# Kernel tuning notes

Measured on AMD Instinct MI355X. Metric: run time of the kernel, lower is better.

## Reference

```python
import jax, jax.numpy as jnp
import numpy as np

B, N, E, T = 32768, 6, 6, 2  # batch graphs, nodes, edges (ring), edge types
H, DIN = 128, 3


def _ring_rel():
    # off_diag[i, (i+1)%N] = 1 -> edge e: sender i, receiver (i+1)%N
    send = np.arange(N)
    recv = (np.arange(N) + 1) % N
    eye = np.eye(N, dtype=np.float32)
    return jnp.asarray(eye[recv]), jnp.asarray(eye[send])  # rel_rec, rel_send [E,N]


def setup_inputs() -> dict:
    key = jax.random.key(0)
    ks = iter(jax.random.split(key, 40))
    rn = lambda shape, s=0.1: jax.random.normal(next(ks), shape, jnp.float32) * s
    rel_rec, rel_send = _ring_rel()
    inp = {
        'x': rn((B, N, DIN), 1.0),
        'rel_rec': rel_rec, 'rel_send': rel_send,
        'e1w1': rn((DIN, H)), 'e1b1': jnp.full((H,), 0.1), 'e1w2': rn((H, H)), 'e1b2': jnp.full((H,), 0.1),
        'e2w1': rn((2 * H, H)), 'e2b1': jnp.full((H,), 0.1), 'e2w2': rn((H, H)), 'e2b2': jnp.full((H,), 0.1),
        'e3w1': rn((H, H)), 'e3b1': jnp.full((H,), 0.1), 'e3w2': rn((H, H)), 'e3b2': jnp.full((H,), 0.1),
        'e4w1': rn((2 * H, H)), 'e4b1': jnp.full((H,), 0.1), 'e4w2': rn((H, H)), 'e4b2': jnp.full((H,), 0.1),
        'ew_out': rn((H, T)), 'eb_out': jnp.full((T,), 0.1),
        'd_msg_w1': rn((T, 2 * DIN, H)), 'd_msg_b1': rn((T, H), 0.01),
        'd_msg_w2': rn((T, H, H)), 'd_msg_b2': rn((T, H), 0.01),
        'd_out_w1': rn((DIN + H, H)), 'd_out_b1': rn((H,), 0.01),
        'd_out_w2': rn((H, H)), 'd_out_b2': rn((H,), 0.01),
        'd_out_w3': rn((H, DIN)), 'd_out_b3': rn((DIN,), 0.01),
    }
    return inp


def _mlp(h, w1, b1, w2, b2):
    # two-layer ELU MLP (dropout inactive at eval)
    return jax.nn.elu(jax.nn.elu(h @ w1 + b1) @ w2 + b2)


def reference(x, rel_rec, rel_send,
              e1w1, e1b1, e1w2, e1b2, e2w1, e2b1, e2w2, e2b2,
              e3w1, e3b1, e3w2, e3b2, e4w1, e4b1, e4w2, e4b2,
              ew_out, eb_out,
              d_msg_w1, d_msg_b1, d_msg_w2, d_msg_b2,
              d_out_w1, d_out_b1, d_out_w2, d_out_b2, d_out_w3, d_out_b3):
    node2edge = lambda h: jnp.concatenate(
        [jnp.einsum('en,bnh->beh', rel_rec, h), jnp.einsum('en,bnh->beh', rel_send, h)], axis=-1)

    # ---- GraphEncoder (factor=False) ----
    h = _mlp(x, e1w1, e1b1, e1w2, e1b2)                      # [B,N,H]
    he = _mlp(node2edge(h), e2w1, e2b1, e2w2, e2b2)          # [B,E,H]
    h2 = _mlp(he, e3w1, e3b1, e3w2, e3b2)                    # [B,E,H]
    h3 = _mlp(jnp.concatenate([h2, he], -1), e4w1, e4b1, e4w2, e4b2)
    logits = h3 @ ew_out + eb_out                            # [B,E,T]
    rel_type = jax.nn.softmax(logits, axis=-1)               # edge-type weights

    # ---- GraphDecoder single step (skip_first=False) ----
    recv = jnp.einsum('en,bnd->bed', rel_rec, x)             # [B,E,DIN]
    send = jnp.einsum('en,bnd->bed', rel_send, x)
    pre_msg = jnp.concatenate([recv, send], axis=-1)         # [B,E,2*DIN]
    # batched per-edge-type MLP: one grouped GEMM instead of a python loop of layers
    m = jax.nn.relu(jnp.einsum('bei,tih->bteh', pre_msg, d_msg_w1) + d_msg_b1[None, :, None, :])
    m = jax.nn.relu(jnp.einsum('bteh,tho->bteo', m, d_msg_w2) + d_msg_b2[None, :, None, :])
    all_msgs = jnp.einsum('bteh,bet->beh', m, rel_type)      # weight + accumulate over types
    agg_msgs = jnp.einsum('beh,en->bnh', all_msgs, rel_rec)  # edge -> node aggregation

    aug = jnp.concatenate([x, agg_msgs], axis=-1)            # [B,N,DIN+H]
    p = jax.nn.relu(aug @ d_out_w1 + d_out_b1)
    p = jax.nn.relu(p @ d_out_w2 + d_out_b2)
    p = p @ d_out_w3 + d_out_b3
    return x + p                                             # [B,N,DIN]
```

## Files before the change

kernel.cpp:

```cpp
#include <hip/hip_runtime.h>
#include <hip/hip_bf16.h>

typedef __bf16 bf16x8 __attribute__((ext_vector_type(8)));
typedef __bf16 bf16x4 __attribute__((ext_vector_type(4)));
typedef float floatx4 __attribute__((ext_vector_type(4)));

#define LDW 136
#define PXW 8

#define O_E1W2  0
#define O_E2W1  16384
#define O_E2W2  49152
#define O_E3W1  65536
#define O_E3W2  81920
#define O_E4W1  98304
#define O_E4W2  131072
#define O_DM2T0 147456
#define O_DM2T1 163840
#define O_DO1   180224
#define O_DO2   196608
#define O_EWOUT 212992
#define O_DW3   215040
#define O_E1W1P 217088
#define O_M1T0P 221184
#define O_M1T1P 225280
#define O_DO1XP 229376
#define WS_ELEMS 233472

__global__ void prep_kernel(const float* e1w2, const float* e2w1, const float* e2w2,
    const float* e3w1, const float* e3w2, const float* e4w1, const float* e4w2,
    const float* dmsg2, const float* dout1, const float* dout2,
    const float* ew_out, const float* dout_w3, const float* e1w1,
    const float* dmsg_w1, __hip_bfloat16* ws) {
  int idx = blockIdx.x * 256 + threadIdx.x;
  if (idx >= WS_ELEMS) return;
  float v;
  if (idx < O_E2W1)      { int l = idx;           v = e1w2[(l & 127) * 128 + (l >> 7)]; }
  else if (idx < O_E2W2) { int l = idx - O_E2W1;  v = e2w1[(l & 255) * 128 + (l >> 8)]; }
  else if (idx < O_E3W1) { int l = idx - O_E2W2;  v = e2w2[(l & 127) * 128 + (l >> 7)]; }
  else if (idx < O_E3W2) { int l = idx - O_E3W1;  v = e3w1[(l & 127) * 128 + (l >> 7)]; }
  else if (idx < O_E4W1) { int l = idx - O_E3W2;  v = e3w2[(l & 127) * 128 + (l >> 7)]; }
  else if (idx < O_E4W2) { int l = idx - O_E4W1;  v = e4w1[(l & 255) * 128 + (l >> 8)]; }
  else if (idx < O_DM2T0){ int l = idx - O_E4W2;  v = e4w2[(l & 127) * 128 + (l >> 7)]; }
  else if (idx < O_DM2T1){ int l = idx - O_DM2T0; v = dmsg2[(l & 127) * 128 + (l >> 7)]; }
  else if (idx < O_DO1)  { int l = idx - O_DM2T1; v = dmsg2[16384 + (l & 127) * 128 + (l >> 7)]; }
  else if (idx < O_DO2)  { int l = idx - O_DO1;   v = dout1[384 + (l & 127) * 128 + (l >> 7)]; }
  else if (idx < O_EWOUT){ int l = idx - O_DO2;   v = dout2[(l & 127) * 128 + (l >> 7)]; }
  else if (idx < O_DW3)  { int l = idx - O_EWOUT; int n = l >> 7;
                           v = (n < 2) ? ew_out[(l & 127) * 2 + n] : 0.f; }
  else if (idx < O_E1W1P){ int l = idx - O_DW3;   int n = l >> 7;
                           v = (n < 3) ? dout_w3[(l & 127) * 3 + n] : 0.f; }
  else if (idx < O_M1T0P){ int l = idx - O_E1W1P; int n = l >> 5, c = l & 31;
                           v = (c >= 3 && c < 6) ? e1w1[(c - 3) * 128 + n] : 0.f; }
  else if (idx < O_M1T1P){ int l = idx - O_M1T0P; int n = l >> 5, c = l & 31;
                           v = (c < 6) ? dmsg_w1[c * 128 + n] : 0.f; }
  else if (idx < O_DO1XP){ int l = idx - O_M1T1P; int n = l >> 5, c = l & 31;
                           v = (c < 6) ? dmsg_w1[768 + c * 128 + n] : 0.f; }
  else                   { int l = idx - O_DO1XP; int n = l >> 5, c = l & 31;
                           v = (c >= 3 && c < 6) ? dout1[(c - 3) * 128 + n] : 0.f; }
  ws[idx] = __float2bfloat16(v);
}

struct W4 { bf16x8 b[4]; };
struct W8 { bf16x8 b[8]; };
union PK { bf16x4 v; __hip_bfloat16 h[4]; };

__global__ __launch_bounds__(512, 4) void nri_fused(
    const float* __restrict__ x,
    const float* __restrict__ e1b1, const float* __restrict__ e1b2,
    const float* __restrict__ e2b1, const float* __restrict__ e2b2,
    const float* __restrict__ e3b1, const float* __restrict__ e3b2,
    const float* __restrict__ e4b1, const float* __restrict__ e4b2,
    const float* __restrict__ eb_out,
    const float* __restrict__ dmsg_b1, const float* __restrict__ dmsg_b2,
    const float* __restrict__ dout_b1, const float* __restrict__ dout_b2,
    const float* __restrict__ dout_b3,
    const __bf16* __restrict__ wt, float* __restrict__ out)
{
  const int tid  = threadIdx.x;
  const int wave = tid >> 6;
  const int lane = tid & 63;
  const int nl   = lane & 15;
  const int quad = lane >> 4;
  const int colb = wave * 16 + nl;
  const int cq   = wave * 16 + quad * 4;
  const int gx   = blockIdx.x * 288;

  __shared__ __align__(16) __hip_bfloat16 bufA[96 * LDW];
  __shared__ __align__(16) __hip_bfloat16 bufB[96 * LDW];
  __shared__ __align__(16) __hip_bfloat16 pxb[96 * PXW];
  __shared__ __hip_bfloat16 rtw[192];

  floatx4 b_s1 = *(const floatx4*)(e1b1 + cq);
  bf16x8 wk_s1 = *(const bf16x8*)(wt + O_E1W1P + colb * 32 + quad * 8);

  for (int i = tid; i < 96 * PXW; i += 512) {
    int row = i >> 3, c = i & 7;
    int e = row % 6;
    float v = 0.f;
    if (c < 3)      { int rr = row + ((e == 5) ? -5 : 1); v = x[gx + rr * 3 + c]; }
    else if (c < 6) v = x[gx + row * 3 + (c - 3)];
    pxb[i] = __float2bfloat16(v);
  }
  __syncthreads();

  auto initv = [&](floatx4 (&a)[6], floatx4 bv) {
#pragma unroll
    for (int mt = 0; mt < 6; ++mt) a[mt] = bv;
  };

  auto loadW128 = [&](int wofs) {
    W4 w;
    const __bf16* p = wt + wofs + colb * 128 + quad * 8;
#pragma unroll
    for (int ks = 0; ks < 4; ++ks) w.b[ks] = *(const bf16x8*)(p + ks * 32);
    return w;
  };
  auto loadW256 = [&](int wofs) {
    W8 w;
    const __bf16* p = wt + wofs + colb * 256 + quad * 8;
#pragma unroll
    for (int ks = 0; ks < 8; ++ks) w.b[ks] = *(const bf16x8*)(p + ks * 32);
    return w;
  };
  auto loadW256half = [&](int wofs, int kh) {
    W4 w;
    const __bf16* p = wt + wofs + colb * 256 + kh * 128 + quad * 8;
#pragma unroll
    for (int ks = 0; ks < 4; ++ks) w.b[ks] = *(const bf16x8*)(p + ks * 32);
    return w;
  };

  auto gemmP = [&](floatx4 (&acc)[6], const W4& w, const __hip_bfloat16* in) {
    const __bf16* ab = (const __bf16*)(const void*)in;
#pragma unroll
    for (int ks = 0; ks < 4; ++ks) {
      int kk = ks * 32 + quad * 8;
#pragma unroll
      for (int mt = 0; mt < 6; ++mt) {
        bf16x8 b = *(const bf16x8*)(ab + (mt * 16 + nl) * LDW + kk);
        acc[mt] = __builtin_amdgcn_mfma_f32_16x16x32_bf16(w.b[ks], b, acc[mt], 0, 0, 0);
      }
    }
  };
  auto gemmP2 = [&](floatx4 (&accA)[6], const W4& wA, floatx4 (&accB)[6],
                    const W4& wB, const __hip_bfloat16* in) {
    const __bf16* ab = (const __bf16*)(const void*)in;
#pragma unroll
    for (int ks = 0; ks < 4; ++ks) {
      int kk = ks * 32 + quad * 8;
#pragma unroll
      for (int mt = 0; mt < 6; ++mt) {
        bf16x8 b = *(const bf16x8*)(ab + (mt * 16 + nl) * LDW + kk);
        accA[mt] = __builtin_amdgcn_mfma_f32_16x16x32_bf16(wA.b[ks], b, accA[mt], 0, 0, 0);
        accB[mt] = __builtin_amdgcn_mfma_f32_16x16x32_bf16(wB.b[ks], b, accB[mt], 0, 0, 0);
      }
    }
  };
  auto gemm256P = [&](floatx4 (&acc)[6], const W8& w, const __hip_bfloat16* in) {
    int rofs0[6], rofs1[6];
#pragma unroll
    for (int mt = 0; mt < 6; ++mt) {
      int r = mt * 16 + nl;
      rofs1[mt] = r * LDW;
      int e = r % 6;
      rofs0[mt] = (r + ((e == 5) ? -5 : 1)) * LDW;
    }
    const __bf16* ab = (const __bf16*)(const void*)in;
#pragma unroll
    for (int ks = 0; ks < 8; ++ks) {
      int kk = (ks & 3) * 32 + quad * 8;
      const int* rofs = (ks < 4) ? rofs0 : rofs1;
#pragma unroll
      for (int mt = 0; mt < 6; ++mt) {
        bf16x8 b = *(const bf16x8*)(ab + rofs[mt] + kk);
        acc[mt] = __builtin_amdgcn_mfma_f32_16x16x32_bf16(w.b[ks], b, acc[mt], 0, 0, 0);
      }
    }
  };
  auto gemm32 = [&](floatx4 (&acc)[6], bf16x8 wfrag) {
    const __bf16* pb = (const __bf16*)(const void*)pxb;
#pragma unroll
    for (int mt = 0; mt < 6; ++mt) {
      bf16x8 b = {0, 0, 0, 0, 0, 0, 0, 0};
      if (quad == 0) b = *(const bf16x8*)(pb + (mt * 16 + nl) * PXW);
      acc[mt] = __builtin_amdgcn_mfma_f32_16x16x32_bf16(wfrag, b, acc[mt], 0, 0, 0);
    }
  };
  auto store_act = [&](floatx4 (&acc)[6], int act, __hip_bfloat16* ob) {
#pragma unroll
    for (int mt = 0; mt < 6; ++mt) {
      PK p;
#pragma unroll
      for (int r = 0; r < 4; ++r) {
        float z = acc[mt][r];
        if (act == 1) z = (z > 0.f) ? z : (__expf(z) - 1.f);
        else z = fmaxf(z, 0.f);
        p.h[r] = __float2bfloat16(z);
      }
      *(bf16x4*)((__bf16*)(void*)ob + (mt * 16 + nl) * LDW + cq) = p.v;
    }
  };

  floatx4 acc[6], acc2[6];

  initv(acc, b_s1); gemm32(acc, wk_s1);
  W4 w2 = loadW128(O_E1W2);
  floatx4 b_s2 = *(const floatx4*)(e1b2 + cq);
  store_act(acc, 1, bufA);
  __syncthreads();
  initv(acc, b_s2); gemmP(acc, w2, bufA);
  W8 w3 = loadW256(O_E2W1);
  floatx4 b_s3 = *(const floatx4*)(e2b1 + cq);
  store_act(acc, 1, bufB);
  __syncthreads();
  initv(acc, b_s3); gemm256P(acc, w3, bufB);
  W4 w4 = loadW128(O_E2W2);
  floatx4 b_s4 = *(const floatx4*)(e2b2 + cq);
  store_act(acc, 1, bufA);
  __syncthreads();
  initv(acc, b_s4); gemmP(acc, w4, bufA);
  W4 w5 = loadW128(O_E3W1);
  W4 w5b = loadW256half(O_E4W1, 1);
  floatx4 b_s5 = *(const floatx4*)(e3b1 + cq);
  floatx4 b2_s5 = *(const floatx4*)(e4b1 + cq);
  store_act(acc, 1, bufB);
  __syncthreads();
  initv(acc, b_s5); initv(acc2, b2_s5);
  gemmP2(acc, w5, acc2, w5b, bufB);
  W4 w6 = loadW128(O_E3W2);
  floatx4 b_s6 = *(const floatx4*)(e3b2 + cq);
  store_act(acc, 1, bufA);
  __syncthreads();
  initv(acc, b_s6); gemmP(acc, w6, bufA);
  W4 w7 = loadW256half(O_E4W1, 0);
  store_act(acc, 1, bufB);
  __syncthreads();
  gemmP(acc2, w7, bufB);
  W4 w8 = loadW128(O_E4W2);
  floatx4 b_s8 = *(const floatx4*)(e4b2 + cq);
  store_act(acc2, 1, bufA);
  __syncthreads();
  initv(acc, b_s8); gemmP(acc, w8, bufA);
  float ebv = (nl < 2) ? eb_out[nl] : 0.f;
  bf16x8 wk10a = *(const bf16x8*)(wt + O_M1T0P + colb * 32 + quad * 8);
  bf16x8 wk10b = *(const bf16x8*)(wt + O_M1T1P + colb * 32 + quad * 8);
  floatx4 b_m0 = *(const floatx4*)(dmsg_b1 + cq);
  floatx4 b_m1 = *(const floatx4*)(dmsg_b1 + 128 + cq);
  store_act(acc, 1, bufB);
  __syncthreads();

  if (wave < 6) {
    int tile = wave;
    floatx4 lg = {ebv, ebv, ebv, ebv};
    const __bf16* ab = (const __bf16*)(const void*)bufB;
    const __bf16* wp = wt + O_EWOUT + nl * 128 + quad * 8;
#pragma unroll
    for (int ks = 0; ks < 4; ++ks) {
      bf16x8 a = *(const bf16x8*)(ab + (tile * 16 + nl) * LDW + ks * 32 + quad * 8);
      bf16x8 b = *(const bf16x8*)(wp + ks * 32);
      lg = __builtin_amdgcn_mfma_f32_16x16x32_bf16(a, b, lg, 0, 0, 0);
    }
    if (nl < 2) {
#pragma unroll
      for (int r = 0; r < 4; ++r)
        rtw[(tile * 16 + quad * 4 + r) * 2 + nl] = __float2bfloat16(lg[r]);
    }
  }
  __syncthreads();

  if (tid < 96) {
    float l0 = __bfloat162float(rtw[tid * 2]);
    float l1 = __bfloat162float(rtw[tid * 2 + 1]);
    float mx = fmaxf(l0, l1);
    float ea = __expf(l0 - mx), eb = __expf(l1 - mx);
    float inv = 1.f / (ea + eb);
    rtw[tid * 2] = __float2bfloat16(ea * inv);
    rtw[tid * 2 + 1] = __float2bfloat16(eb * inv);
  }
  initv(acc, b_m0);  gemm32(acc, wk10a);  store_act(acc, 2, bufA);
  initv(acc2, b_m1); gemm32(acc2, wk10b); store_act(acc2, 2, bufB);
  W4 wm0 = loadW128(O_DM2T0);
  W4 wm1 = loadW128(O_DM2T1);
  floatx4 b_d0 = *(const floatx4*)(dmsg_b2 + cq);
  floatx4 b_d1 = *(const floatx4*)(dmsg_b2 + 128 + cq);
  __syncthreads();

  initv(acc, b_d0);  gemmP(acc, wm0, bufA);
  initv(acc2, b_d1); gemmP(acc2, wm1, bufB);
#pragma unroll
  for (int mt = 0; mt < 6; ++mt) {
    int row = mt * 16 + nl;
    float r0 = __bfloat162float(rtw[row * 2]);
    float r1 = __bfloat162float(rtw[row * 2 + 1]);
#pragma unroll
    for (int r = 0; r < 4; ++r)
      acc[mt][r] = r0 * fmaxf(acc[mt][r], 0.f) + r1 * fmaxf(acc2[mt][r], 0.f);
  }
  W4 wd1 = loadW128(O_DO1);
  bf16x8 wk13 = *(const bf16x8*)(wt + O_DO1XP + colb * 32 + quad * 8);
  floatx4 b_p1 = *(const floatx4*)(dout_b1 + cq);
  __syncthreads();

#pragma unroll
  for (int mt = 0; mt < 6; ++mt) {
    int row = mt * 16 + nl;
    int e = row % 6;
    int orow = row + ((e == 5) ? -5 : 1);
    PK p;
#pragma unroll
    for (int r = 0; r < 4; ++r) p.h[r] = __float2bfloat16(acc[mt][r]);
    *(bf16x4*)((__bf16*)(void*)bufA + orow * LDW + cq) = p.v;
  }
  __syncthreads();

  initv(acc, b_p1); gemmP(acc, wd1, bufA); gemm32(acc, wk13);
  W4 wd2 = loadW128(O_DO2);
  floatx4 b_p2 = *(const floatx4*)(dout_b2 + cq);
  store_act(acc, 2, bufB);
  __syncthreads();
  initv(acc, b_p2); gemmP(acc, wd2, bufB);
  float b3v = (nl < 3) ? dout_b3[nl] : 0.f;
  store_act(acc, 2, bufA);
  __syncthreads();

  if (wave < 6) {
    int tile = wave;
    floatx4 d = {b3v, b3v, b3v, b3v};
    const __bf16* ab = (const __bf16*)(const void*)bufA;
    const __bf16* wp = wt + O_DW3 + nl * 128 + quad * 8;
#pragma unroll
    for (int ks = 0; ks < 4; ++ks) {
      bf16x8 a = *(const bf16x8*)(ab + (tile * 16 + nl) * LDW + ks * 32 + quad * 8);
      bf16x8 b = *(const bf16x8*)(wp + ks * 32);
      d = __builtin_amdgcn_mfma_f32_16x16x32_bf16(a, b, d, 0, 0, 0);
    }
    if (nl < 3) {
#pragma unroll
      for (int r = 0; r < 4; ++r) {
        int row = tile * 16 + quad * 4 + r;
        out[gx + row * 3 + nl] = x[gx + row * 3 + nl] + d[r];
      }
    }
  }
}

extern "C" void kernel_launch(void* const* d_in, const int* in_sizes, int n_in,
                              void* d_out, int out_size, void* d_ws, size_t ws_size,
                              hipStream_t stream) {
  const float* x       = (const float*)d_in[0];
  const float* e1w1    = (const float*)d_in[3];
  const float* e1b1    = (const float*)d_in[4];
  const float* e1w2    = (const float*)d_in[5];
  const float* e1b2    = (const float*)d_in[6];
  const float* e2w1    = (const float*)d_in[7];
  const float* e2b1    = (const float*)d_in[8];
  const float* e2w2    = (const float*)d_in[9];
  const float* e2b2    = (const float*)d_in[10];
  const float* e3w1    = (const float*)d_in[11];
  const float* e3b1    = (const float*)d_in[12];
  const float* e3w2    = (const float*)d_in[13];
  const float* e3b2    = (const float*)d_in[14];
  const float* e4w1    = (const float*)d_in[15];
  const float* e4b1    = (const float*)d_in[16];
  const float* e4w2    = (const float*)d_in[17];
  const float* e4b2    = (const float*)d_in[18];
  const float* ew_out  = (const float*)d_in[19];
  const float* eb_out  = (const float*)d_in[20];
  const float* dmsg_w1 = (const float*)d_in[21];
  const float* dmsg_b1 = (const float*)d_in[22];
  const float* dmsg_w2 = (const float*)d_in[23];
  const float* dmsg_b2 = (const float*)d_in[24];
  const float* dout_w1 = (const float*)d_in[25];
  const float* dout_b1 = (const float*)d_in[26];
  const float* dout_w2 = (const float*)d_in[27];
  const float* dout_b2 = (const float*)d_in[28];
  const float* dout_w3 = (const float*)d_in[29];
  const float* dout_b3 = (const float*)d_in[30];

  prep_kernel<<<(WS_ELEMS + 255) / 256, 256, 0, stream>>>(
      e1w2, e2w1, e2w2, e3w1, e3w2, e4w1, e4w2, dmsg_w2, dout_w1, dout_w2,
      ew_out, dout_w3, e1w1, dmsg_w1, (__hip_bfloat16*)d_ws);

  nri_fused<<<32768 / 16, 512, 0, stream>>>(
      x, e1b1, e1b2, e2b1, e2b2, e3b1, e3b2, e4b1, e4b2, eb_out,
      dmsg_b1, dmsg_b2, dout_b1, dout_b2, dout_b3,
      (const __bf16*)d_ws, (float*)d_out);
}
```

Measured before the change: 257.0 us.

## Restructure fused NRI kernel so each wave processes two graphs independently

```diff
diff --git a/kernel.cpp b/kernel.cpp
--- a/kernel.cpp
+++ b/kernel.cpp
@@ -61,11 +61,9 @@
   ws[idx] = __float2bfloat16(v);
 }
 
-struct W4 { bf16x8 b[4]; };
-struct W8 { bf16x8 b[8]; };
 union PK { bf16x4 v; __hip_bfloat16 h[4]; };
 
-__global__ __launch_bounds__(512, 4) void nri_fused(
+__global__ __launch_bounds__(256, 4) void nri_fused(
     const float* __restrict__ x,
     const float* __restrict__ e1b1, const float* __restrict__ e1b2,
     const float* __restrict__ e2b1, const float* __restrict__ e2b2,
@@ -82,265 +80,211 @@
   const int lane = tid & 63;
   const int nl   = lane & 15;
   const int quad = lane >> 4;
-  const int colb = wave * 16 + nl;
-  const int cq   = wave * 16 + quad * 4;
-  const int gx   = blockIdx.x * 288;
-
-  __shared__ __align__(16) __hip_bfloat16 bufA[96 * LDW];
-  __shared__ __align__(16) __hip_bfloat16 bufB[96 * LDW];
-  __shared__ __align__(16) __hip_bfloat16 pxb[96 * PXW];
-  __shared__ __hip_bfloat16 rtw[192];
-
-  floatx4 b_s1 = *(const floatx4*)(e1b1 + cq);
-  bf16x8 wk_s1 = *(const bf16x8*)(wt + O_E1W1P + colb * 32 + quad * 8);
-
-  for (int i = tid; i < 96 * PXW; i += 512) {
+  const int gw   = blockIdx.x * 4 + wave;
+  const int gxw  = gw * 36;
+  const int rsh  = (nl >= 12) ? nl : ((nl % 6 == 5) ? nl - 5 : nl + 1);
+
+  __shared__ __align__(16) __hip_bfloat16 tAs[4][16 * LDW];
+  __shared__ __align__(16) __hip_bfloat16 tBs[4][16 * LDW];
+  __shared__ __align__(16) __hip_bfloat16 pxs[4][16 * PXW];
+  __shared__ __hip_bfloat16 rts[4][32];
+
+  __hip_bfloat16* tA  = tAs[wave];
+  __hip_bfloat16* tB  = tBs[wave];
+  __hip_bfloat16* pxw = pxs[wave];
+  __hip_bfloat16* rtw = rts[wave];
+
+#pragma unroll
+  for (int it = 0; it < 2; ++it) {
+    int i = lane + it * 64;
     int row = i >> 3, c = i & 7;
-    int e = row % 6;
     float v = 0.f;
-    if (c < 3)      { int rr = row + ((e == 5) ? -5 : 1); v = x[gx + rr * 3 + c]; }
-    else if (c < 6) v = x[gx + row * 3 + (c - 3)];
-    pxb[i] = __float2bfloat16(v);
-  }
-  __syncthreads();
-
-  auto initv = [&](floatx4 (&a)[6], floatx4 bv) {
-#pragma unroll
-    for (int mt = 0; mt < 6; ++mt) a[mt] = bv;
-  };
-
-  auto loadW128 = [&](int wofs) {
-    W4 w;
-    const __bf16* p = wt + wofs + colb * 128 + quad * 8;
-#pragma unroll
-    for (int ks = 0; ks < 4; ++ks) w.b[ks] = *(const bf16x8*)(p + ks * 32);
-    return w;
-  };
-  auto loadW256 = [&](int wofs) {
-    W8 w;
-    const __bf16* p = wt + wofs + colb * 256 + quad * 8;
-#pragma unroll
-    for (int ks = 0; ks < 8; ++ks) w.b[ks] = *(const bf16x8*)(p + ks * 32);
-    return w;
-  };
-  auto loadW256half = [&](int wofs, int kh) {
-    W4 w;
-    const __bf16* p = wt + wofs + colb * 256 + kh * 128 + quad * 8;
-#pragma unroll
-    for (int ks = 0; ks < 4; ++ks) w.b[ks] = *(const bf16x8*)(p + ks * 32);
-    return w;
-  };
-
-  auto gemmP = [&](floatx4 (&acc)[6], const W4& w, const __hip_bfloat16* in) {
-    const __bf16* ab = (const __bf16*)(const void*)in;
+    if (row < 12 && c < 6) {
+      int rr = (c < 3) ? ((row % 6 == 5) ? row - 5 : row + 1) : row;
+      v = x[gxw + rr * 3 + (c < 3 ? c : c - 3)];
+    }
+    pxw[i] = __float2bfloat16(v);
+  }
+
+  auto bfrags = [&](const __hip_bfloat16* tp, bf16x8 (&bf)[4], int row) {
+    const __bf16* p = (const __bf16*)(const void*)tp + row * LDW + quad * 8;
+#pragma unroll
+    for (int ks = 0; ks < 4; ++ks) bf[ks] = *(const bf16x8*)(p + ks * 32);
+  };
+  auto ldbias = [&](floatx4 (&acc)[8], const float* b, int ofs) {
+#pragma unroll
+    for (int ct = 0; ct < 8; ++ct)
+      acc[ct] = *(const floatx4*)(b + ofs + ct * 16 + quad * 4);
+  };
+  auto gemmW = [&](floatx4 (&acc)[8], int wofs, const bf16x8 (&bf)[4]) {
 #pragma unroll
     for (int ks = 0; ks < 4; ++ks) {
-      int kk = ks * 32 + quad * 8;
-#pragma unroll
-      for (int mt = 0; mt < 6; ++mt) {
-        bf16x8 b = *(const bf16x8*)(ab + (mt * 16 + nl) * LDW + kk);
-        acc[mt] = __builtin_amdgcn_mfma_f32_16x16x32_bf16(w.b[ks], b, acc[mt], 0, 0, 0);
+#pragma unroll
+      for (int ct = 0; ct < 8; ++ct) {
+        bf16x8 a = *(const bf16x8*)(wt + wofs + (ct * 16 + nl) * 128 + ks * 32 + quad * 8);
+        acc[ct] = __builtin_amdgcn_mfma_f32_16x16x32_bf16(a, bf[ks], acc[ct], 0, 0, 0);
       }
     }
   };
-  auto gemmP2 = [&](floatx4 (&accA)[6], const W4& wA, floatx4 (&accB)[6],
-                    const W4& wB, const __hip_bfloat16* in) {
-    const __bf16* ab = (const __bf16*)(const void*)in;
+  auto gemmW256h = [&](floatx4 (&acc)[8], int wofs, int kh, const bf16x8 (&bf)[4]) {
 #pragma unroll
     for (int ks = 0; ks < 4; ++ks) {
-      int kk = ks * 32 + quad * 8;
-#pragma unroll
-      for (int mt = 0; mt < 6; ++mt) {
-        bf16x8 b = *(const bf16x8*)(ab + (mt * 16 + nl) * LDW + kk);
-        accA[mt] = __builtin_amdgcn_mfma_f32_16x16x32_bf16(wA.b[ks], b, accA[mt], 0, 0, 0);
-        accB[mt] = __builtin_amdgcn_mfma_f32_16x16x32_bf16(wB.b[ks], b, accB[mt], 0, 0, 0);
+#pragma unroll
+      for (int ct = 0; ct < 8; ++ct) {
+        bf16x8 a = *(const bf16x8*)(wt + wofs + (ct * 16 + nl) * 256 + kh * 128 + ks * 32 + quad * 8);
+        acc[ct] = __builtin_amdgcn_mfma_f32_16x16x32_bf16(a, bf[ks], acc[ct], 0, 0, 0);
       }
     }
   };
-  auto gemm256P = [&](floatx4 (&acc)[6], const W8& w, const __hip_bfloat16* in) {
-    int rofs0[6], rofs1[6];
-#pragma unroll
-    for (int mt = 0; mt < 6; ++mt) {
-      int r = mt * 16 + nl;
-      rofs1[mt] = r * LDW;
-      int e = r % 6;
-      rofs0[mt] = (r + ((e == 5) ? -5 : 1)) * LDW;
-    }
-    const __bf16* ab = (const __bf16*)(const void*)in;
-#pragma unroll
-    for (int ks = 0; ks < 8; ++ks) {
-      int kk = (ks & 3) * 32 + quad * 8;
-      const int* rofs = (ks < 4) ? rofs0 : rofs1;
-#pragma unroll
-      for (int mt = 0; mt < 6; ++mt) {
-        bf16x8 b = *(const bf16x8*)(ab + rofs[mt] + kk);
-        acc[mt] = __builtin_amdgcn_mfma_f32_16x16x32_bf16(w.b[ks], b, acc[mt], 0, 0, 0);
-      }
-    }
-  };
-  auto gemm32 = [&](floatx4 (&acc)[6], bf16x8 wfrag) {
-    const __bf16* pb = (const __bf16*)(const void*)pxb;
-#pragma unroll
-    for (int mt = 0; mt < 6; ++mt) {
-      bf16x8 b = {0, 0, 0, 0, 0, 0, 0, 0};
-      if (quad == 0) b = *(const bf16x8*)(pb + (mt * 16 + nl) * PXW);
-      acc[mt] = __builtin_amdgcn_mfma_f32_16x16x32_bf16(wfrag, b, acc[mt], 0, 0, 0);
-    }
-  };
-  auto store_act = [&](floatx4 (&acc)[6], int act, __hip_bfloat16* ob) {
-#pragma unroll
-    for (int mt = 0; mt < 6; ++mt) {
+  auto gemm32 = [&](floatx4 (&acc)[8], int wofs) {
+    bf16x8 b = {0, 0, 0, 0, 0, 0, 0, 0};
+    if (quad == 0)
+      b = *(const bf16x8*)((const __bf16*)(const void*)pxw + nl * PXW);
+#pragma unroll
+    for (int ct = 0; ct < 8; ++ct) {
+      bf16x8 a = *(const bf16x8*)(wt + wofs + (ct * 16 + nl) * 32 + quad * 8);
+      acc[ct] = __builtin_amdgcn_mfma_f32_16x16x32_bf16(a, b, acc[ct], 0, 0, 0);
+    }
+  };
+  auto store_act = [&](floatx4 (&acc)[8], int act, __hip_bfloat16* tp, int row) {
+#pragma unroll
+    for (int ct = 0; ct < 8; ++ct) {
       PK p;
 #pragma unroll
       for (int r = 0; r < 4; ++r) {
-        float z = acc[mt][r];
+        float z = acc[ct][r];
         if (act == 1) z = (z > 0.f) ? z : (__expf(z) - 1.f);
-        else z = fmaxf(z, 0.f);
+        else if (act == 2) z = fmaxf(z, 0.f);
         p.h[r] = __float2bfloat16(z);
       }
-      *(bf16x4*)((__bf16*)(void*)ob + (mt * 16 + nl) * LDW + cq) = p.v;
-    }
-  };
-
-  floatx4 acc[6], acc2[6];
-
-  initv(acc, b_s1); gemm32(acc, wk_s1);
-  W4 w2 = loadW128(O_E1W2);
-  floatx4 b_s2 = *(const floatx4*)(e1b2 + cq);
-  store_act(acc, 1, bufA);
-  __syncthreads();
-  initv(acc, b_s2); gemmP(acc, w2, bufA);
-  W8 w3 = loadW256(O_E2W1);
-  floatx4 b_s3 = *(const floatx4*)(e2b1 + cq);
-  store_act(acc, 1, bufB);
-  __syncthreads();
-  initv(acc, b_s3); gemm256P(acc, w3, bufB);
-  W4 w4 = loadW128(O_E2W2);
-  floatx4 b_s4 = *(const floatx4*)(e2b2 + cq);
-  store_act(acc, 1, bufA);
-  __syncthreads();
-  initv(acc, b_s4); gemmP(acc, w4, bufA);
-  W4 w5 = loadW128(O_E3W1);
-  W4 w5b = loadW256half(O_E4W1, 1);
-  floatx4 b_s5 = *(const floatx4*)(e3b1 + cq);
-  floatx4 b2_s5 = *(const floatx4*)(e4b1 + cq);
-  store_act(acc, 1, bufB);
-  __syncthreads();
-  initv(acc, b_s5); initv(acc2, b2_s5);
-  gemmP2(acc, w5, acc2, w5b, bufB);
-  W4 w6 = loadW128(O_E3W2);
-  floatx4 b_s6 = *(const floatx4*)(e3b2 + cq);
-  store_act(acc, 1, bufA);
-  __syncthreads();
-  initv(acc, b_s6); gemmP(acc, w6, bufA);
-  W4 w7 = loadW256half(O_E4W1, 0);
-  store_act(acc, 1, bufB);
-  __syncthreads();
-  gemmP(acc2, w7, bufB);
-  W4 w8 = loadW128(O_E4W2);
-  floatx4 b_s8 = *(const floatx4*)(e4b2 + cq);
-  store_act(acc2, 1, bufA);
-  __syncthreads();
-  initv(acc, b_s8); gemmP(acc, w8, bufA);
-  float ebv = (nl < 2) ? eb_out[nl] : 0.f;
-  bf16x8 wk10a = *(const bf16x8*)(wt + O_M1T0P + colb * 32 + quad * 8);
-  bf16x8 wk10b = *(const bf16x8*)(wt + O_M1T1P + colb * 32 + quad * 8);
-  floatx4 b_m0 = *(const floatx4*)(dmsg_b1 + cq);
-  floatx4 b_m1 = *(const floatx4*)(dmsg_b1 + 128 + cq);
-  store_act(acc, 1, bufB);
-  __syncthreads();
-
-  if (wave < 6) {
-    int tile = wave;
-    floatx4 lg = {ebv, ebv, ebv, ebv};
-    const __bf16* ab = (const __bf16*)(const void*)bufB;
-    const __bf16* wp = wt + O_EWOUT + nl * 128 + quad * 8;
+      *(bf16x4*)((__bf16*)(void*)tp + row * LDW + ct * 16 + quad * 4) = p.v;
+    }
+  };
+
+  floatx4 acc[8], acc2[8];
+  bf16x8 bf[4];
+
+  ldbias(acc, e1b1, 0);
+  gemm32(acc, O_E1W1P);
+  store_act(acc, 1, tA, nl);
+
+  ldbias(acc, e1b2, 0);
+  bfrags(tA, bf, nl);
+  gemmW(acc, O_E1W2, bf);
+  store_act(acc, 1, tB, nl);
+
+  ldbias(acc, e2b1, 0);
+  bfrags(tB, bf, rsh);
+#pragma unroll
+  for (int ks = 0; ks < 4; ++ks) {
+#pragma unroll
+    for (int ct = 0; ct < 8; ++ct) {
+      bf16x8 a = *(const bf16x8*)(wt + O_E2W1 + (ct * 16 + nl) * 256 + ks * 32 + quad * 8);
+      acc[ct] = __builtin_amdgcn_mfma_f32_16x16x32_bf16(a, bf[ks], acc[ct], 0, 0, 0);
+    }
+  }
+  bfrags(tB, bf, nl);
+#pragma unroll
+  for (int ks = 0; ks < 4; ++ks) {
+#pragma unroll
+    for (int ct = 0; ct < 8; ++ct) {
+      bf16x8 a = *(const bf16x8*)(wt + O_E2W1 + (ct * 16 + nl) * 256 + 128 + ks * 32 + quad * 8);
+      acc[ct] = __builtin_amdgcn_mfma_f32_16x16x32_bf16(a, bf[ks], acc[ct], 0, 0, 0);
+    }
+  }
+  store_act(acc, 1, tA, nl);
+
+  ldbias(acc, e2b2, 0);
+  bfrags(tA, bf, nl);
+  gemmW(acc, O_E2W2, bf);
+  store_act(acc, 1, tB, nl);
+
+  ldbias(acc, e3b1, 0);
+  ldbias(acc2, e4b1, 0);
+  bfrags(tB, bf, nl);
+  gemmW(acc, O_E3W1, bf);
+  gemmW256h(acc2, O_E4W1, 1, bf);
+  store_act(acc, 1, tA, nl);
+
+  ldbias(acc, e3b2, 0);
+  bfrags(tA, bf, nl);
+  gemmW(acc, O_E3W2, bf);
+  store_act(acc, 1, tB, nl);
+
+  bfrags(tB, bf, nl);
+  gemmW256h(acc2, O_E4W1, 0, bf);
+  store_act(acc2, 1, tA, nl);
+
+  ldbias(acc, e4b2, 0);
+  bfrags(tA, bf, nl);
+  gemmW(acc, O_E4W2, bf);
+  store_act(acc, 1, tB, nl);
+
+  {
+    floatx4 lg = {eb_out[0], eb_out[1], 0.f, 0.f};
+    bfrags(tB, bf, nl);
 #pragma unroll
     for (int ks = 0; ks < 4; ++ks) {
-      bf16x8 a = *(const bf16x8*)(ab + (tile * 16 + nl) * LDW + ks * 32 + quad * 8);
-      bf16x8 b = *(const bf16x8*)(wp + ks * 32);
-      lg = __builtin_amdgcn_mfma_f32_16x16x32_bf16(a, b, lg, 0, 0, 0);
-    }
-    if (nl < 2) {
+      bf16x8 a = *(const bf16x8*)(wt + O_EWOUT + nl * 128 + ks * 32 + quad * 8);
+      lg = __builtin_amdgcn_mfma_f32_16x16x32_bf16(a, bf[ks], lg, 0, 0, 0);
+    }
+    if (quad == 0) {
+      float l0 = lg[0], l1 = lg[1];
+      float mx = fmaxf(l0, l1);
+      float ea = __expf(l0 - mx), ebx = __expf(l1 - mx);
+      float inv = 1.f / (ea + ebx);
+      rtw[nl * 2]     = __float2bfloat16(ea * inv);
+      rtw[nl * 2 + 1] = __float2bfloat16(ebx * inv);
+    }
+  }
+
+  ldbias(acc, dmsg_b1, 0);
+  gemm32(acc, O_M1T0P);
+  store_act(acc, 2, tA, nl);
+  ldbias(acc2, dmsg_b1, 128);
+  gemm32(acc2, O_M1T1P);
+  store_act(acc2, 2, tB, nl);
+
+  ldbias(acc, dmsg_b2, 0);
+  bfrags(tA, bf, nl);
+  gemmW(acc, O_DM2T0, bf);
+  ldbias(acc2, dmsg_b2, 128);
+  bfrags(tB, bf, nl);
+  gemmW(acc2, O_DM2T1, bf);
+  {
+    float r0 = __bfloat162float(rtw[nl * 2]);
+    float r1 = __bfloat162float(rtw[nl * 2 + 1]);
+#pragma unroll
+    for (int ct = 0; ct < 8; ++ct)
 #pragma unroll
       for (int r = 0; r < 4; ++r)
-        rtw[(tile * 16 + quad * 4 + r) * 2 + nl] = __float2bfloat16(lg[r]);
-    }
-  }
-  __syncthreads();
-
-  if (tid < 96) {
-    float l0 = __bfloat162float(rtw[tid * 2]);
-    float l1 = __bfloat162float(rtw[tid * 2 + 1]);
-    float mx = fmaxf(l0, l1);
-    float ea = __expf(l0 - mx), eb = __expf(l1 - mx);
-    float inv = 1.f / (ea + eb);
-    rtw[tid * 2] = __float2bfloat16(ea * inv);
-    rtw[tid * 2 + 1] = __float2bfloat16(eb * inv);
-  }
-  initv(acc, b_m0);  gemm32(acc, wk10a);  store_act(acc, 2, bufA);
-  initv(acc2, b_m1); gemm32(acc2, wk10b); store_act(acc2, 2, bufB);
-  W4 wm0 = loadW128(O_DM2T0);
-  W4 wm1 = loadW128(O_DM2T1);
-  floatx4 b_d0 = *(const floatx4*)(dmsg_b2 + cq);
-  floatx4 b_d1 = *(const floatx4*)(dmsg_b2 + 128 + cq);
-  __syncthreads();
-
-  initv(acc, b_d0);  gemmP(acc, wm0, bufA);
-  initv(acc2, b_d1); gemmP(acc2, wm1, bufB);
-#pragma unroll
-  for (int mt = 0; mt < 6; ++mt) {
-    int row = mt * 16 + nl;
-    float r0 = __bfloat162float(rtw[row * 2]);
-    float r1 = __bfloat162float(rtw[row * 2 + 1]);
-#pragma unroll
-    for (int r = 0; r < 4; ++r)
-      acc[mt][r] = r0 * fmaxf(acc[mt][r], 0.f) + r1 * fmaxf(acc2[mt][r], 0.f);
-  }
-  W4 wd1 = loadW128(O_DO1);
-  bf16x8 wk13 = *(const bf16x8*)(wt + O_DO1XP + colb * 32 + quad * 8);
-  floatx4 b_p1 = *(const floatx4*)(dout_b1 + cq);
-  __syncthreads();
-
-#pragma unroll
-  for (int mt = 0; mt < 6; ++mt) {
-    int row = mt * 16 + nl;
-    int e = row % 6;
-    int orow = row + ((e == 5) ? -5 : 1);
-    PK p;
-#pragma unroll
-    for (int r = 0; r < 4; ++r) p.h[r] = __float2bfloat16(acc[mt][r]);
-    *(bf16x4*)((__bf16*)(void*)bufA + orow * LDW + cq) = p.v;
-  }
-  __syncthreads();
-
-  initv(acc, b_p1); gemmP(acc, wd1, bufA); gemm32(acc, wk13);
-  W4 wd2 = loadW128(O_DO2);
-  floatx4 b_p2 = *(const floatx4*)(dout_b2 + cq);
-  store_act(acc, 2, bufB);
-  __syncthreads();
-  initv(acc, b_p2); gemmP(acc, wd2, bufB);
-  float b3v = (nl < 3) ? dout_b3[nl] : 0.f;
-  store_act(acc, 2, bufA);
-  __syncthreads();
-
-  if (wave < 6) {
-    int tile = wave;
-    floatx4 d = {b3v, b3v, b3v, b3v};
-    const __bf16* ab = (const __bf16*)(const void*)bufA;
-    const __bf16* wp = wt + O_DW3 + nl * 128 + quad * 8;
+        acc[ct][r] = r0 * fmaxf(acc[ct][r], 0.f) + r1 * fmaxf(acc2[ct][r], 0.f);
+  }
+  store_act(acc, 0, tA, rsh);
+
+  ldbias(acc, dout_b1, 0);
+  bfrags(tA, bf, nl);
+  gemmW(acc, O_DO1, bf);
+  gemm32(acc, O_DO1XP);
+  store_act(acc, 2, tB, nl);
+
+  ldbias(acc, dout_b2, 0);
+  bfrags(tB, bf, nl);
+  gemmW(acc, O_DO2, bf);
+  store_act(acc, 2, tA, nl);
+
+  {
+    floatx4 d = {dout_b3[0], dout_b3[1], dout_b3[2], 0.f};
+    bfrags(tA, bf, nl);
 #pragma unroll
     for (int ks = 0; ks < 4; ++ks) {
-      bf16x8 a = *(const bf16x8*)(ab + (tile * 16 + nl) * LDW + ks * 32 + quad * 8);
-      bf16x8 b = *(const bf16x8*)(wp + ks * 32);
-      d = __builtin_amdgcn_mfma_f32_16x16x32_bf16(a, b, d, 0, 0, 0);
-    }
-    if (nl < 3) {
-#pragma unroll
-      for (int r = 0; r < 4; ++r) {
-        int row = tile * 16 + quad * 4 + r;
-        out[gx + row * 3 + nl] = x[gx + row * 3 + nl] + d[r];
-      }
+      bf16x8 a = *(const bf16x8*)(wt + O_DW3 + nl * 128 + ks * 32 + quad * 8);
+      d = __builtin_amdgcn_mfma_f32_16x16x32_bf16(a, bf[ks], d, 0, 0, 0);
+    }
+    if (quad == 0 && nl < 12) {
+#pragma unroll
+      for (int r = 0; r < 3; ++r)
+        out[gxw + nl * 3 + r] = x[gxw + nl * 3 + r] + d[r];
     }
   }
 }
@@ -382,7 +326,7 @@
       e1w2, e2w1, e2w2, e3w1, e3w2, e4w1, e4w2, dmsg_w2, dout_w1, dout_w2,
       ew_out, dout_w3, e1w1, dmsg_w1, (__hip_bfloat16*)d_ws);
 
-  nri_fused<<<32768 / 16, 512, 0, stream>>>(
+  nri_fused<<<32768 / 8, 256, 0, stream>>>(
       x, e1b1, e1b2, e2b1, e2b2, e3b1, e3b2, e4b1, e4b2, eb_out,
       dmsg_b1, dmsg_b2, dout_b1, dout_b2, dout_b3,
       (const __bf16*)d_ws, (float*)d_out);
```

New measurement: 986.1 us. 284% more time.
